# Performance work log

Hardware: AMD Instinct MI355X
Metric: run time of the kernel (lower is better)

## Reference

```python
import jax, jax.numpy as jnp
import numpy as np


def setup_inputs() -> dict:
    key = jax.random.key(0)
    k1, k2, k3 = jax.random.split(key, 3)
    B, C, D, S = 16, 80, 1024, 14  # batch, num_classes, feature dim, conv size
    return {
        "batch_size": B,
        "img_feature_map": jax.random.normal(k1, (B, D, S, S), dtype=jnp.float32),
        "word_features": jax.random.normal(k2, (C, D), dtype=jnp.float32),
        "fc_a_w": jax.random.normal(k3, (D,), dtype=jnp.float32) / np.float32(np.sqrt(D)),
        "fc_a_b": jnp.zeros((), dtype=jnp.float32),
    }


def reference(batch_size, img_feature_map, word_features, fc_a_w, fc_a_b):
    # img_feature_map: [B, D, H, W] -> [B, H, W, D]
    img = jnp.transpose(img_feature_map, (0, 2, 3, 1))
    # class-wise gated feature: tanh(img * word) -> [B, H, W, C, D]
    gated = jnp.tanh(img[:, :, :, None, :] * word_features[None, None, None, :, :])
    # rank-1 linear score: [B, H, W, C]
    scores = jnp.einsum('bhwcd,d->bhwc', gated, fc_a_w) + fc_a_b
    B, H, W, C = scores.shape
    # softmax over spatial positions (H*W) per (batch, class)
    coef = jax.nn.softmax(scores.reshape(B, H * W, C), axis=1).reshape(B, H, W, C)
    # attention-weighted spatial pooling -> [B, C, D]
    return jnp.einsum('bhwc,bhwd->bcd', coef, img)
```

## Files before the change

kernel.cpp:

```cpp
#include <hip/hip_runtime.h>

#define BB 16
#define CC 80
#define DD 1024
#define HW 196
#define NSP (BB * HW)
#define NCH 8
#define DCH 128
#define CPB 8
#define NCQ (CC / CPB)
#define PG 16
#define TWO_LOG2E 2.8853900817779268f

__global__ __launch_bounds__(256) void scores_k(const float* __restrict__ img,
                                                const float* __restrict__ word,
                                                const float* __restrict__ fa,
                                                float* __restrict__ partial,
                                                float* __restrict__ imgT) {
    const int g = blockIdx.x * 256 + threadIdx.x;
    if (g >= NSP) return;
    const int b  = g / HW;
    const int hw = g - b * HW;
    const int d0 = blockIdx.y * DCH;
    const int c0 = blockIdx.z * CPB;

    const float* ip = img + ((size_t)b * DD + d0) * HW + hw;

    float p[CPB];
#pragma unroll
    for (int k = 0; k < CPB; ++k) p[k] = 0.f;

    for (int q = 0; q < DCH / 32; ++q) {
        float iv[32];
        const float* qp = ip + (size_t)q * 32 * HW;
#pragma unroll
        for (int i = 0; i < 32; ++i)
            iv[i] = qp[(size_t)i * HW];

        if (blockIdx.z == 0) {
            float4* tp = (float4*)(imgT + (size_t)g * DD + d0 + q * 32);
#pragma unroll
            for (int i = 0; i < 8; ++i)
                tp[i] = make_float4(iv[4 * i], iv[4 * i + 1], iv[4 * i + 2], iv[4 * i + 3]);
        }

#pragma unroll
        for (int i = 0; i < 32; ++i)
            iv[i] *= TWO_LOG2E;

        const float* fp = fa + d0 + q * 32;
#pragma unroll
        for (int k = 0; k < CPB; ++k) {
            const float* wp = word + (size_t)(c0 + k) * DD + d0 + q * 32;
            float p0 = 0.f, p1 = 0.f;
#pragma unroll
            for (int i = 0; i < 32; i += 2) {
                float y0 = iv[i]     * wp[i];
                float y1 = iv[i + 1] * wp[i + 1];
                float e0 = __builtin_amdgcn_exp2f(y0);
                float e1 = __builtin_amdgcn_exp2f(y1);
                float r0 = __builtin_amdgcn_rcpf(e0 + 1.f);
                float r1 = __builtin_amdgcn_rcpf(e1 + 1.f);
                p0 = fmaf(fp[i],     r0, p0);
                p1 = fmaf(fp[i + 1], r1, p1);
            }
            p[k] += p0 + p1;
        }
    }

#pragma unroll
    for (int k = 0; k < CPB; ++k)
        partial[(((size_t)b * NCH + blockIdx.y) * CC + (c0 + k)) * HW + hw]
            = (-TWO_LOG2E) * p[k];
}

__global__ __launch_bounds__(256) void softmax_k(float* __restrict__ partial) {
    const int bc = blockIdx.x;
    const int b = bc / CC, c = bc - b * CC;
    const int t = threadIdx.x;

    float x = -3.4e38f;
    if (t < HW) {
        float P = 0.f;
#pragma unroll
        for (int ch = 0; ch < NCH; ++ch)
            P += partial[(((size_t)b * NCH + ch) * CC + c) * HW + t];
        x = P;
    }

    __shared__ float rmax[4], rsum[4];
    const int wv = t >> 6;

    float m = x;
#pragma unroll
    for (int off = 32; off >= 1; off >>= 1) m = fmaxf(m, __shfl_xor(m, off, 64));
    if ((t & 63) == 0) rmax[wv] = m;
    __syncthreads();
    m = fmaxf(fmaxf(rmax[0], rmax[1]), fmaxf(rmax[2], rmax[3]));

    float e = (t < HW) ? __builtin_amdgcn_exp2f(x - m) : 0.f;
    float s = e;
#pragma unroll
    for (int off = 32; off >= 1; off >>= 1) s += __shfl_xor(s, off, 64);
    if ((t & 63) == 0) rsum[wv] = s;
    __syncthreads();
    s = rsum[0] + rsum[1] + rsum[2] + rsum[3];

    if (t < HW)
        partial[((size_t)b * NCH * CC + c) * HW + t] = e * __builtin_amdgcn_rcpf(s);
}

__global__ __launch_bounds__(256) void pool4_k(const float* __restrict__ imgT,
                                               const float* __restrict__ partial,
                                               float* __restrict__ out) {
    __shared__ float ct[PG * HW];
    const int b  = blockIdx.x;
    const int d0 = blockIdx.y * 128;
    const int cg = blockIdx.z * PG;
    const int t  = threadIdx.x;
    const int w  = t >> 6, l = t & 63;

    const float4* cs = (const float4*)(partial + ((size_t)b * NCH * CC + cg) * HW);
    float4* cd = (float4*)ct;
    for (int j = t; j < PG * HW / 4; j += 256) cd[j] = cs[j];
    __syncthreads();

    const float* ib  = imgT + (size_t)b * HW * DD + d0 + 2 * l;
    const float* cr0 = ct + (4 * w) * HW;

    float2 a0 = {0, 0}, a1 = {0, 0}, a2 = {0, 0}, a3 = {0, 0};
    for (int h = 0; h < HW; h += 4) {
        float2 i0 = *(const float2*)(ib + (size_t)(h    ) * DD);
        float2 i1 = *(const float2*)(ib + (size_t)(h + 1) * DD);
        float2 i2 = *(const float2*)(ib + (size_t)(h + 2) * DD);
        float2 i3 = *(const float2*)(ib + (size_t)(h + 3) * DD);
        float4 c0v = *(const float4*)(cr0 + h);
        float4 c1v = *(const float4*)(cr0 + HW + h);
        float4 c2v = *(const float4*)(cr0 + 2 * HW + h);
        float4 c3v = *(const float4*)(cr0 + 3 * HW + h);
#define ACC2(A, CV)                                                              \
        A.x = fmaf(CV.x, i0.x, fmaf(CV.y, i1.x, fmaf(CV.z, i2.x, fmaf(CV.w, i3.x, A.x)))); \
        A.y = fmaf(CV.x, i0.y, fmaf(CV.y, i1.y, fmaf(CV.z, i2.y, fmaf(CV.w, i3.y, A.y))));
        ACC2(a0, c0v)
        ACC2(a1, c1v)
        ACC2(a2, c2v)
        ACC2(a3, c3v)
#undef ACC2
    }

    float* ob = out + ((size_t)b * CC + cg + 4 * w) * DD + d0 + 2 * l;
    *(float2*)(ob)                  = a0;
    *(float2*)(ob + DD)             = a1;
    *(float2*)(ob + 2 * (size_t)DD) = a2;
    *(float2*)(ob + 3 * (size_t)DD) = a3;
}

extern "C" void kernel_launch(void* const* d_in, const int* in_sizes, int n_in,
                              void* d_out, int out_size, void* d_ws, size_t ws_size,
                              hipStream_t stream) {
    const float* img  = (const float*)d_in[1];
    const float* word = (const float*)d_in[2];
    const float* fa   = (const float*)d_in[3];
    float* out = (float*)d_out;

    float* partial = (float*)d_ws;
    float* imgT    = partial + (size_t)BB * NCH * CC * HW;

    scores_k<<<dim3((NSP + 255) / 256, NCH, NCQ), 256, 0, stream>>>(img, word, fa, partial, imgT);
    softmax_k<<<BB * CC, 256, 0, stream>>>(partial);
    pool4_k<<<dim3(BB, NCH, CC / PG), 256, 0, stream>>>(imgT, partial, out);
}
```

Before: 169.7 us.

## Double-buffer image loads in scores kernel, halve classes per block, narrow pool tiles

The scores kernel now handles 4 classes per block instead of 8, which doubles the grid in z. Its four D-quarter iterations are unrolled into a manual ping-pong between two register buffers, with sched_barriers so the loads of the next quarter are issued before the current one is computed. The pooling kernel processes 64 D columns per block with scalar loads instead of 128 with float2, doubling its grid to improve occupancy and latency hiding. In exchange, the scores kernel rereads the image twice as often across class blocks and uses more registers for the second buffer.

```diff
diff --git a/kernel.cpp b/kernel.cpp
--- a/kernel.cpp
+++ b/kernel.cpp
@@ -7,7 +7,7 @@
 #define NSP (BB * HW)
 #define NCH 8
 #define DCH 128
-#define CPB 8
+#define CPB 4
 #define NCQ (CC / CPB)
 #define PG 16
 #define TWO_LOG2E 2.8853900817779268f
@@ -23,6 +23,7 @@
     const int hw = g - b * HW;
     const int d0 = blockIdx.y * DCH;
     const int c0 = blockIdx.z * CPB;
+    const bool zz = (blockIdx.z == 0);
 
     const float* ip = img + ((size_t)b * DD + d0) * HW + hw;
 
@@ -30,20 +31,21 @@
 #pragma unroll
     for (int k = 0; k < CPB; ++k) p[k] = 0.f;
 
-    for (int q = 0; q < DCH / 32; ++q) {
-        float iv[32];
+    float ivA[32], ivB[32];
+
+    auto loadq = [&](float* iv, int q) {
         const float* qp = ip + (size_t)q * 32 * HW;
 #pragma unroll
         for (int i = 0; i < 32; ++i)
             iv[i] = qp[(size_t)i * HW];
-
-        if (blockIdx.z == 0) {
+    };
+    auto computeq = [&](float* iv, int q) {
+        if (zz) {
             float4* tp = (float4*)(imgT + (size_t)g * DD + d0 + q * 32);
 #pragma unroll
             for (int i = 0; i < 8; ++i)
                 tp[i] = make_float4(iv[4 * i], iv[4 * i + 1], iv[4 * i + 2], iv[4 * i + 3]);
         }
-
 #pragma unroll
         for (int i = 0; i < 32; ++i)
             iv[i] *= TWO_LOG2E;
@@ -66,7 +68,20 @@
             }
             p[k] += p0 + p1;
         }
-    }
+    };
+
+    loadq(ivA, 0);
+    __builtin_amdgcn_sched_barrier(0);
+    loadq(ivB, 1);
+    __builtin_amdgcn_sched_barrier(0);
+    computeq(ivA, 0);
+    loadq(ivA, 2);
+    __builtin_amdgcn_sched_barrier(0);
+    computeq(ivB, 1);
+    loadq(ivB, 3);
+    __builtin_amdgcn_sched_barrier(0);
+    computeq(ivA, 2);
+    computeq(ivB, 3);
 
 #pragma unroll
     for (int k = 0; k < CPB; ++k)
@@ -110,12 +125,12 @@
         partial[((size_t)b * NCH * CC + c) * HW + t] = e * __builtin_amdgcn_rcpf(s);
 }
 
-__global__ __launch_bounds__(256) void pool4_k(const float* __restrict__ imgT,
+__global__ __launch_bounds__(256) void pool5_k(const float* __restrict__ imgT,
                                                const float* __restrict__ partial,
                                                float* __restrict__ out) {
     __shared__ float ct[PG * HW];
     const int b  = blockIdx.x;
-    const int d0 = blockIdx.y * 128;
+    const int d0 = blockIdx.y * 64;
     const int cg = blockIdx.z * PG;
     const int t  = threadIdx.x;
     const int w  = t >> 6, l = t & 63;
@@ -125,34 +140,30 @@
     for (int j = t; j < PG * HW / 4; j += 256) cd[j] = cs[j];
     __syncthreads();
 
-    const float* ib  = imgT + (size_t)b * HW * DD + d0 + 2 * l;
+    const float* ib  = imgT + (size_t)b * HW * DD + d0 + l;
     const float* cr0 = ct + (4 * w) * HW;
 
-    float2 a0 = {0, 0}, a1 = {0, 0}, a2 = {0, 0}, a3 = {0, 0};
+    float a0 = 0.f, a1 = 0.f, a2 = 0.f, a3 = 0.f;
     for (int h = 0; h < HW; h += 4) {
-        float2 i0 = *(const float2*)(ib + (size_t)(h    ) * DD);
-        float2 i1 = *(const float2*)(ib + (size_t)(h + 1) * DD);
-        float2 i2 = *(const float2*)(ib + (size_t)(h + 2) * DD);
-        float2 i3 = *(const float2*)(ib + (size_t)(h + 3) * DD);
+        float i0 = ib[(size_t)(h    ) * DD];
+        float i1 = ib[(size_t)(h + 1) * DD];
+        float i2 = ib[(size_t)(h + 2) * DD];
+        float i3 = ib[(size_t)(h + 3) * DD];
         float4 c0v = *(const float4*)(cr0 + h);
         float4 c1v = *(const float4*)(cr0 + HW + h);
         float4 c2v = *(const float4*)(cr0 + 2 * HW + h);
         float4 c3v = *(const float4*)(cr0 + 3 * HW + h);
-#define ACC2(A, CV)                                                              \
-        A.x = fmaf(CV.x, i0.x, fmaf(CV.y, i1.x, fmaf(CV.z, i2.x, fmaf(CV.w, i3.x, A.x)))); \
-        A.y = fmaf(CV.x, i0.y, fmaf(CV.y, i1.y, fmaf(CV.z, i2.y, fmaf(CV.w, i3.y, A.y))));
-        ACC2(a0, c0v)
-        ACC2(a1, c1v)
-        ACC2(a2, c2v)
-        ACC2(a3, c3v)
-#undef ACC2
+        a0 = fmaf(c0v.x, i0, fmaf(c0v.y, i1, fmaf(c0v.z, i2, fmaf(c0v.w, i3, a0))));
+        a1 = fmaf(c1v.x, i0, fmaf(c1v.y, i1, fmaf(c1v.z, i2, fmaf(c1v.w, i3, a1))));
+        a2 = fmaf(c2v.x, i0, fmaf(c2v.y, i1, fmaf(c2v.z, i2, fmaf(c2v.w, i3, a2))));
+        a3 = fmaf(c3v.x, i0, fmaf(c3v.y, i1, fmaf(c3v.z, i2, fmaf(c3v.w, i3, a3))));
     }
 
-    float* ob = out + ((size_t)b * CC + cg + 4 * w) * DD + d0 + 2 * l;
-    *(float2*)(ob)                  = a0;
-    *(float2*)(ob + DD)             = a1;
-    *(float2*)(ob + 2 * (size_t)DD) = a2;
-    *(float2*)(ob + 3 * (size_t)DD) = a3;
+    float* ob = out + ((size_t)b * CC + cg + 4 * w) * DD + d0 + l;
+    ob[0]              = a0;
+    ob[DD]             = a1;
+    ob[2 * (size_t)DD] = a2;
+    ob[3 * (size_t)DD] = a3;
 }
 
 extern "C" void kernel_launch(void* const* d_in, const int* in_sizes, int n_in,
@@ -168,5 +179,5 @@
 
     scores_k<<<dim3((NSP + 255) / 256, NCH, NCQ), 256, 0, stream>>>(img, word, fa, partial, imgT);
     softmax_k<<<BB * CC, 256, 0, stream>>>(partial);
-    pool4_k<<<dim3(BB, NCH, CC / PG), 256, 0, stream>>>(imgT, partial, out);
+    pool5_k<<<dim3(BB, DD / 64, CC / PG), 256, 0, stream>>>(imgT, partial, out);
 }
```

After: 167.5 us. About the same (-1.3%).
